# Performance work log

Measured on AMD Instinct MI355X. Metric: run time of the kernel, lower is better.

The kernel has to match this reference:

```python
import jax, jax.numpy as jnp
import numpy as np

B, T, D, U = 32, 1024, 512, 512

def hard_sigmoid(x):
    # Keras hard_sigmoid: clip(0.2*x + 0.5, 0, 1)
    return jnp.clip(x * 0.2 + 0.5, 0.0, 1.0)

def setup_inputs() -> dict:
    key = jax.random.key(0)
    k1, k2, k3 = jax.random.split(key, 3)
    x = jax.random.normal(k1, (B, T, D), dtype=jnp.float32)
    kernel = jax.random.normal(k2, (D, 4 * U), dtype=jnp.float32) * 0.02
    recurrent_kernel = jax.random.normal(k3, (U, 4 * U), dtype=jnp.float32) * 0.02
    # unit_forget_bias: forget-gate slice initialized to 1
    bias = jnp.zeros((4 * U,), dtype=jnp.float32).at[U:2 * U].set(1.0)
    return {"x": x, "kernel": kernel, "recurrent_kernel": recurrent_kernel, "bias": bias}

def reference(x, kernel, recurrent_kernel, bias):
    units = recurrent_kernel.shape[0]
    batch = x.shape[0]
    # Precompute input projections for all timesteps in one big GEMM
    # (implementation=2 style): [B, T, 4U]
    xz = jnp.einsum('btd,dg->btg', x, kernel) + bias
    xz_t = jnp.transpose(xz, (1, 0, 2))  # [T, B, 4U]

    h0 = jnp.zeros((batch, units), dtype=x.dtype)
    c0 = jnp.zeros((batch, units), dtype=x.dtype)

    def step(carry, z_x):
        h, c = carry
        z = z_x + h @ recurrent_kernel  # [B, 4U]
        zi, zf, zc, zo = jnp.split(z, 4, axis=-1)
        i = hard_sigmoid(zi)
        f = hard_sigmoid(zf)
        c_new = f * c + i * jnp.tanh(zc)
        o = hard_sigmoid(zo)
        h_new = o * jnp.tanh(c_new)
        return (h_new, c_new), h_new

    (_, _), hs = jax.lax.scan(step, (h0, c0), xz_t)  # hs: [T, B, U]
    return jnp.transpose(hs, (1, 0, 2))  # [B, T, U] (return_sequences=True)
```

## Files before the change

### kernel.cpp

```cpp
#include <hip/hip_runtime.h>


#define TT 1024
#define DD 512
#define UU 512
#define NCOL 2048
#define SENT 0xFFFFFFFFu
#define RDEPTH 4

typedef float f32x2 __attribute__((ext_vector_type(2)));
typedef float f32x4 __attribute__((ext_vector_type(4)));
typedef unsigned int u32x4 __attribute__((ext_vector_type(4)));

__device__ __forceinline__ float hsig(float v) {
  return fminf(fmaxf(0.2f * v + 0.5f, 0.0f), 1.0f);
}
__device__ __forceinline__ float tanh_fast(float x) {
  float e = __expf(2.0f * x);
  return 1.0f - 2.0f / (e + 1.0f);
}

template <bool SLEEP>
__device__ __forceinline__ void wavebar(int* ctr, int& ep) {
  asm volatile("s_waitcnt lgkmcnt(0)" ::: "memory");
  if ((threadIdx.x & 63) == 0)
    __hip_atomic_fetch_add(ctr, 1, __ATOMIC_RELAXED, __HIP_MEMORY_SCOPE_WORKGROUP);
  ep += 4;
  while (__hip_atomic_load(ctr, __ATOMIC_RELAXED, __HIP_MEMORY_SCOPE_WORKGROUP) < ep) {
    if (SLEEP) __builtin_amdgcn_s_sleep(1);
  }
  asm volatile("" ::: "memory");
}

__global__ __launch_bounds__(512, 2) void lstm_persistent(
    const float* __restrict__ x,
    const float* __restrict__ Wk,
    const float* __restrict__ Wr,
    const float* __restrict__ bias,
    float* __restrict__ out) {
  const int tid = (int)threadIdx.x;
  const int g   = (int)blockIdx.x & 7;
  const int w   = (int)blockIdx.x >> 3;
  const bool crit = (tid < 256);
  const int l   = tid & 63;

  __shared__ float LX[8][4][65];
  __shared__ float LR[2][8][4][66];
  __shared__ float RING[RDEPTH][4][66];
  __shared__ float LH[4][8][68];
  __shared__ float LB[64];
  __shared__ int cXZdone, cCRITdone, cXZbar, cCRITbar;

  if (tid == 0) { cXZdone = 0; cCRITdone = 0; cXZbar = 0; cCRITbar = 0; }
  if (tid < 64) LB[tid] = bias[(tid >> 4) * UU + w * 16 + (tid & 15)];

  f32x2 W2[64];
  {
    const int wv  = tid >> 6;
    const int idx = tid & 255;
    const int cp  = crit ? (l & 31) : (idx & 31);
    const int ko  = crit ? (2 * (wv & 3) + (l >> 5)) : (idx >> 5);
    const int gcb = (cp >> 3) * UU + w * 16 + ((2 * cp) & 15);
    const float* M = crit ? Wr : Wk;
#pragma unroll
    for (int j = 0; j < 64; ++j)
      W2[j] = *(const f32x2*)(M + (size_t)(64 * ko + j) * NCOL + gcb);
  }
  __syncthreads();

  if (crit) {
    const int wv   = tid >> 6;
    const int kq0  = 2 * wv;
    const int kql  = kq0 + (l >> 5);
    const int cp   = l & 31;
    const int gsel = l >> 4;
    const int b_p  = l >> 4;
    const int m    = l & 15;
    const unsigned* hb = (const unsigned*)out +
        (size_t)(g * 4 + b_p) * TT * UU + 128 * wv + 8 * m;
    float* lhdst = &LH[b_p][kq0 + (m >> 3)][8 * (m & 7)];
    float c_state = 0.0f;
    int epC = 0;

    for (int t = 0; t < TT; ++t) {
      if (t > 0) {
        const unsigned* p = hb + (size_t)(t - 1) * UU;
        u32x4 A, B;
        for (;;) {
          asm volatile(
              "global_load_dwordx4 %0, %2, off sc0 sc1\n\t"
              "global_load_dwordx4 %1, %2, off offset:16 sc0 sc1\n\t"
              "s_waitcnt vmcnt(0)"
              : "=v"(A), "=v"(B) : "v"(p) : "memory");
          int ok = (A.x != SENT) & (A.y != SENT) & (A.z != SENT) & (A.w != SENT) &
                   (B.x != SENT) & (B.y != SENT) & (B.z != SENT) & (B.w != SENT);
          if (__all(ok)) break;
          __builtin_amdgcn_s_sleep(1);
        }
        *(u32x4*)lhdst       = A;
        *(u32x4*)(lhdst + 4) = B;
        asm volatile("s_waitcnt lgkmcnt(0)" ::: "memory");
        __builtin_amdgcn_sched_barrier(0);
        __builtin_amdgcn_s_setprio(1);
        f32x2 a0 = {0.f, 0.f}, a1 = {0.f, 0.f}, a2 = {0.f, 0.f}, a3 = {0.f, 0.f};
#pragma unroll
        for (int j4 = 0; j4 < 16; ++j4) {
          f32x4 h0 = *(const f32x4*)&LH[0][kql][4 * j4];
          f32x4 h1 = *(const f32x4*)&LH[1][kql][4 * j4];
          f32x4 h2 = *(const f32x4*)&LH[2][kql][4 * j4];
          f32x4 h3 = *(const f32x4*)&LH[3][kql][4 * j4];
#pragma unroll
          for (int jj = 0; jj < 4; ++jj) {
            f32x2 wj = W2[4 * j4 + jj];
            a0 += (f32x2){h0[jj], h0[jj]} * wj;
            a1 += (f32x2){h1[jj], h1[jj]} * wj;
            a2 += (f32x2){h2[jj], h2[jj]} * wj;
            a3 += (f32x2){h3[jj], h3[jj]} * wj;
          }
        }
        __builtin_amdgcn_s_setprio(0);
        const int p2 = t & 1;
        *(f32x2*)&LR[p2][kql][0][2 * cp] = a0;
        *(f32x2*)&LR[p2][kql][1][2 * cp] = a1;
        *(f32x2*)&LR[p2][kql][2][2 * cp] = a2;
        *(f32x2*)&LR[p2][kql][3][2 * cp] = a3;
      }
      while (__hip_atomic_load(&cXZdone, __ATOMIC_RELAXED,
                               __HIP_MEMORY_SCOPE_WORKGROUP) < t + 1) {
      }
      asm volatile("" ::: "memory");
      float s = RING[t & (RDEPTH - 1)][wv][l] + LB[l];
      if (l == 0)
        __hip_atomic_fetch_add(&cCRITdone, 1, __ATOMIC_RELAXED,
                               __HIP_MEMORY_SCOPE_WORKGROUP);
      wavebar<false>(&cCRITbar, epC);
      if (t > 0) {
        const int p2 = t & 1;
#pragma unroll
        for (int kq = 0; kq < 8; ++kq) s += LR[p2][kq][wv][l];
      }
      float za  = __shfl_xor(s, 16);
      float zb  = __shfl_xor(s, 32);
      float zc2 = __shfl_xor(za, 32);
      float zi  = gsel == 0 ? s   : gsel == 1 ? za  : gsel == 2 ? zb  : zc2;
      float zf  = gsel == 0 ? za  : gsel == 1 ? s   : gsel == 2 ? zc2 : zb;
      float zc_ = gsel == 0 ? zb  : gsel == 1 ? zc2 : gsel == 2 ? s   : za;
      float zo  = gsel == 0 ? zc2 : gsel == 1 ? zb  : gsel == 2 ? za  : s;
      float gi = hsig(zi);
      float gf = hsig(zf);
      float gc = tanh_fast(zc_);
      float go = hsig(zo);
      c_state = gf * c_state + gi * gc;
      float h = go * tanh_fast(c_state);
      if (gsel == 0) {
        __hip_atomic_store(
            out + ((size_t)(g * 4 + wv) * TT + t) * UU + w * 16 + l, h,
            __ATOMIC_RELAXED, __HIP_MEMORY_SCOPE_AGENT);
      }
    }
  } else {
    const int idx = tid & 255;
    const int o   = idx >> 5;
    const int cp  = idx & 31;
    const float* xb0 = x + (size_t)(g * 4 + 0) * TT * DD + o * 64;
    const float* xb1 = x + (size_t)(g * 4 + 1) * TT * DD + o * 64;
    const float* xb2 = x + (size_t)(g * 4 + 2) * TT * DD + o * 64;
    const float* xb3 = x + (size_t)(g * 4 + 3) * TT * DD + o * 64;
    int epX = 0;

    for (int t = 0; t < TT; ++t) {
      const size_t off = (size_t)t * DD;
      f32x2 a0 = {0.f, 0.f}, a1 = {0.f, 0.f}, a2 = {0.f, 0.f}, a3 = {0.f, 0.f};
#pragma unroll
      for (int j4 = 0; j4 < 16; ++j4) {
        f32x4 v0 = *(const f32x4*)(xb0 + off + 4 * j4);
        f32x4 v1 = *(const f32x4*)(xb1 + off + 4 * j4);
        f32x4 v2 = *(const f32x4*)(xb2 + off + 4 * j4);
        f32x4 v3 = *(const f32x4*)(xb3 + off + 4 * j4);
#pragma unroll
        for (int jj = 0; jj < 4; ++jj) {
          f32x2 wj = W2[4 * j4 + jj];
          a0 += (f32x2){v0[jj], v0[jj]} * wj;
          a1 += (f32x2){v1[jj], v1[jj]} * wj;
          a2 += (f32x2){v2[jj], v2[jj]} * wj;
          a3 += (f32x2){v3[jj], v3[jj]} * wj;
        }
      }
      *(f32x2*)&LX[o][0][2 * cp] = a0;
      *(f32x2*)&LX[o][1][2 * cp] = a1;
      *(f32x2*)&LX[o][2][2 * cp] = a2;
      *(f32x2*)&LX[o][3][2 * cp] = a3;
      wavebar<true>(&cXZbar, epX);
      if (t >= RDEPTH) {
        while (__hip_atomic_load(&cCRITdone, __ATOMIC_RELAXED,
                                 __HIP_MEMORY_SCOPE_WORKGROUP) <
               4 * (t - RDEPTH + 1)) {
          __builtin_amdgcn_s_sleep(1);
        }
        asm volatile("" ::: "memory");
      }
      {
        const int b2 = idx >> 6, c3 = idx & 63;
        float ssum = 0.f;
#pragma unroll
        for (int oo = 0; oo < 8; ++oo) ssum += LX[oo][b2][c3];
        RING[t & (RDEPTH - 1)][b2][c3] = ssum;
      }
      wavebar<true>(&cXZbar, epX);
      if (idx == 0) {
        asm volatile("s_waitcnt lgkmcnt(0)" ::: "memory");
        __hip_atomic_fetch_add(&cXZdone, 1, __ATOMIC_RELAXED,
                               __HIP_MEMORY_SCOPE_WORKGROUP);
      }
    }
  }
}

extern "C" void kernel_launch(void* const* d_in, const int* in_sizes, int n_in,
                              void* d_out, int out_size, void* d_ws, size_t ws_size,
                              hipStream_t stream) {
  const float* x    = (const float*)d_in[0];
  const float* Wk   = (const float*)d_in[1];
  const float* Wr   = (const float*)d_in[2];
  const float* bias = (const float*)d_in[3];
  float* out = (float*)d_out;

  hipMemsetAsync(out, 0xFF, (size_t)out_size * sizeof(float), stream);
  lstm_persistent<<<256, 512, 0, stream>>>(x, Wk, Wr, bias, out);
}
```

Before: 4.792 ms.

## Split batch into two ping-pong halves to overlap h polling with recurrent compute

The four batch rows per block are split into two pairs processed alternately within each timestep, so the global load of one pair's previous hidden state is issued early and overlaps with the other pair's matvec and gate math. Hidden-state polling changes from per-thread dwordx4 loads to scattered dword loads issued ahead and drained with partial vmcnt waits. Gate computation now uses 16 lanes reading four gates directly instead of cross-lane shuffles. The input-projection producer is split per pair with separate counters. The cost is twice as many wave barriers per step and lower lane utilisation in the gate phase.

```diff
diff --git a/kernel.cpp b/kernel.cpp
--- a/kernel.cpp
+++ b/kernel.cpp
@@ -10,7 +10,6 @@
 
 typedef float f32x2 __attribute__((ext_vector_type(2)));
 typedef float f32x4 __attribute__((ext_vector_type(4)));
-typedef unsigned int u32x4 __attribute__((ext_vector_type(4)));
 
 __device__ __forceinline__ float hsig(float v) {
   return fminf(fmaxf(0.2f * v + 0.5f, 0.0f), 1.0f);
@@ -31,6 +30,38 @@
   }
   asm volatile("" ::: "memory");
 }
+
+#define ISSUE4(v0, v1, v2, v3, p0, p1)                                   \
+  asm volatile(                                                          \
+      "global_load_dword %0, %4, off sc0 sc1\n\t"                        \
+      "global_load_dword %1, %4, off offset:256 sc0 sc1\n\t"             \
+      "global_load_dword %2, %5, off sc0 sc1\n\t"                        \
+      "global_load_dword %3, %5, off offset:256 sc0 sc1"                 \
+      : "=v"(v0), "=v"(v1), "=v"(v2), "=v"(v3)                           \
+      : "v"(p0), "v"(p1)                                                 \
+      : "memory")
+
+#define DRAIN4(v0, v1, v2, v3)                                           \
+  asm volatile("s_waitcnt vmcnt(4)"                                      \
+               : "+v"(v0), "+v"(v1), "+v"(v2), "+v"(v3)::"memory")
+
+#define OK4(v0, v1, v2, v3)                                              \
+  ((v0 != SENT) & (v1 != SENT) & (v2 != SENT) & (v3 != SENT))
+
+#define REPOLL4(v0, v1, v2, v3, p0, p1)                                  \
+  for (;;) {                                                             \
+    asm volatile(                                                        \
+        "global_load_dword %0, %4, off sc0 sc1\n\t"                      \
+        "global_load_dword %1, %4, off offset:256 sc0 sc1\n\t"           \
+        "global_load_dword %2, %5, off sc0 sc1\n\t"                      \
+        "global_load_dword %3, %5, off offset:256 sc0 sc1\n\t"           \
+        "s_waitcnt vmcnt(0)"                                             \
+        : "=v"(v0), "=v"(v1), "=v"(v2), "=v"(v3)                         \
+        : "v"(p0), "v"(p1)                                               \
+        : "memory");                                                     \
+    if (__all(OK4(v0, v1, v2, v3))) break;                               \
+    __builtin_amdgcn_s_sleep(1);                                         \
+  }
 
 __global__ __launch_bounds__(512, 2) void lstm_persistent(
     const float* __restrict__ x,
@@ -44,14 +75,15 @@
   const bool crit = (tid < 256);
   const int l   = tid & 63;
 
-  __shared__ float LX[8][4][65];
-  __shared__ float LR[2][8][4][66];
-  __shared__ float RING[RDEPTH][4][66];
-  __shared__ float LH[4][8][68];
+  __shared__ float LX[8][2][66];
+  __shared__ float LR[2][2][8][2][66];
+  __shared__ float RING[2][RDEPTH][2][66];
+  __shared__ float LH[2][2][8][68];
   __shared__ float LB[64];
-  __shared__ int cXZdone, cCRITdone, cXZbar, cCRITbar;
-
-  if (tid == 0) { cXZdone = 0; cCRITdone = 0; cXZbar = 0; cCRITbar = 0; }
+  __shared__ int cXZdone[2], cCRITdone[2], cXZbar, cCRITbar;
+
+  if (tid < 2) { cXZdone[tid] = 0; cCRITdone[tid] = 0; }
+  if (tid == 0) { cXZbar = 0; cCRITbar = 0; }
   if (tid < 64) LB[tid] = bias[(tid >> 4) * UU + w * 16 + (tid & 15)];
 
   f32x2 W2[64];
@@ -73,144 +105,214 @@
     const int kq0  = 2 * wv;
     const int kql  = kq0 + (l >> 5);
     const int cp   = l & 31;
-    const int gsel = l >> 4;
-    const int b_p  = l >> 4;
-    const int m    = l & 15;
-    const unsigned* hb = (const unsigned*)out +
-        (size_t)(g * 4 + b_p) * TT * UU + 128 * wv + 8 * m;
-    float* lhdst = &LH[b_p][kq0 + (m >> 3)][8 * (m & 7)];
+    const int myp  = wv >> 1;
+    const int mybi = wv & 1;
+    const unsigned* oub[2][2];
+#pragma unroll
+    for (int p = 0; p < 2; ++p)
+#pragma unroll
+      for (int bi = 0; bi < 2; ++bi)
+        oub[p][bi] = (const unsigned*)out + (size_t)(g * 4 + 2 * p + bi) * TT * UU;
+    const size_t sl = 128 * wv + l;
     float c_state = 0.0f;
     int epC = 0;
+    unsigned sa0, sa1, sa2, sa3, sb0, sb1, sb2, sb3;
 
     for (int t = 0; t < TT; ++t) {
       if (t > 0) {
-        const unsigned* p = hb + (size_t)(t - 1) * UU;
-        u32x4 A, B;
-        for (;;) {
-          asm volatile(
-              "global_load_dwordx4 %0, %2, off sc0 sc1\n\t"
-              "global_load_dwordx4 %1, %2, off offset:16 sc0 sc1\n\t"
-              "s_waitcnt vmcnt(0)"
-              : "=v"(A), "=v"(B) : "v"(p) : "memory");
-          int ok = (A.x != SENT) & (A.y != SENT) & (A.z != SENT) & (A.w != SENT) &
-                   (B.x != SENT) & (B.y != SENT) & (B.z != SENT) & (B.w != SENT);
-          if (__all(ok)) break;
-          __builtin_amdgcn_s_sleep(1);
-        }
-        *(u32x4*)lhdst       = A;
-        *(u32x4*)(lhdst + 4) = B;
+        const size_t ro = (size_t)(t - 1) * UU + sl;
+        ISSUE4(sb0, sb1, sb2, sb3, oub[1][0] + ro, oub[1][1] + ro);
+      }
+      if (t > 0) {
+        const size_t ro = (size_t)(t - 1) * UU + sl;
+        DRAIN4(sa0, sa1, sa2, sa3);
+        if (!__all(OK4(sa0, sa1, sa2, sa3))) {
+          REPOLL4(sa0, sa1, sa2, sa3, oub[0][0] + ro, oub[0][1] + ro);
+        }
+        LH[0][0][kq0    ][l] = __uint_as_float(sa0);
+        LH[0][0][kq0 + 1][l] = __uint_as_float(sa1);
+        LH[0][1][kq0    ][l] = __uint_as_float(sa2);
+        LH[0][1][kq0 + 1][l] = __uint_as_float(sa3);
         asm volatile("s_waitcnt lgkmcnt(0)" ::: "memory");
         __builtin_amdgcn_sched_barrier(0);
         __builtin_amdgcn_s_setprio(1);
-        f32x2 a0 = {0.f, 0.f}, a1 = {0.f, 0.f}, a2 = {0.f, 0.f}, a3 = {0.f, 0.f};
+        f32x2 a0 = {0.f, 0.f}, a1 = {0.f, 0.f};
 #pragma unroll
         for (int j4 = 0; j4 < 16; ++j4) {
-          f32x4 h0 = *(const f32x4*)&LH[0][kql][4 * j4];
-          f32x4 h1 = *(const f32x4*)&LH[1][kql][4 * j4];
-          f32x4 h2 = *(const f32x4*)&LH[2][kql][4 * j4];
-          f32x4 h3 = *(const f32x4*)&LH[3][kql][4 * j4];
+          f32x4 h0 = *(const f32x4*)&LH[0][0][kql][4 * j4];
+          f32x4 h1 = *(const f32x4*)&LH[0][1][kql][4 * j4];
 #pragma unroll
           for (int jj = 0; jj < 4; ++jj) {
             f32x2 wj = W2[4 * j4 + jj];
             a0 += (f32x2){h0[jj], h0[jj]} * wj;
             a1 += (f32x2){h1[jj], h1[jj]} * wj;
-            a2 += (f32x2){h2[jj], h2[jj]} * wj;
-            a3 += (f32x2){h3[jj], h3[jj]} * wj;
           }
         }
         __builtin_amdgcn_s_setprio(0);
-        const int p2 = t & 1;
-        *(f32x2*)&LR[p2][kql][0][2 * cp] = a0;
-        *(f32x2*)&LR[p2][kql][1][2 * cp] = a1;
-        *(f32x2*)&LR[p2][kql][2][2 * cp] = a2;
-        *(f32x2*)&LR[p2][kql][3][2 * cp] = a3;
-      }
-      while (__hip_atomic_load(&cXZdone, __ATOMIC_RELAXED,
-                               __HIP_MEMORY_SCOPE_WORKGROUP) < t + 1) {
-      }
-      asm volatile("" ::: "memory");
-      float s = RING[t & (RDEPTH - 1)][wv][l] + LB[l];
-      if (l == 0)
-        __hip_atomic_fetch_add(&cCRITdone, 1, __ATOMIC_RELAXED,
-                               __HIP_MEMORY_SCOPE_WORKGROUP);
+        *(f32x2*)&LR[0][t & 1][kql][0][2 * cp] = a0;
+        *(f32x2*)&LR[0][t & 1][kql][1][2 * cp] = a1;
+      }
+      float s0 = 0.f, s1 = 0.f, s2 = 0.f, s3 = 0.f;
+      if (myp == 0 && l < 16) {
+        while (__hip_atomic_load(&cXZdone[0], __ATOMIC_RELAXED,
+                                 __HIP_MEMORY_SCOPE_WORKGROUP) < t + 1) {
+        }
+        asm volatile("" ::: "memory");
+        const int ss = t & (RDEPTH - 1);
+        s0 = RING[0][ss][mybi][l +  0] + LB[l +  0];
+        s1 = RING[0][ss][mybi][l + 16] + LB[l + 16];
+        s2 = RING[0][ss][mybi][l + 32] + LB[l + 32];
+        s3 = RING[0][ss][mybi][l + 48] + LB[l + 48];
+        if (wv == 0 && l == 0) {
+          asm volatile("s_waitcnt lgkmcnt(0)" ::: "memory");
+          __hip_atomic_fetch_add(&cCRITdone[0], 1, __ATOMIC_RELAXED,
+                                 __HIP_MEMORY_SCOPE_WORKGROUP);
+        }
+      }
       wavebar<false>(&cCRITbar, epC);
+      if (myp == 0 && l < 16) {
+        if (t > 0) {
+          const int par = t & 1;
+#pragma unroll
+          for (int kq = 0; kq < 8; ++kq) {
+            s0 += LR[0][par][kq][mybi][l +  0];
+            s1 += LR[0][par][kq][mybi][l + 16];
+            s2 += LR[0][par][kq][mybi][l + 32];
+            s3 += LR[0][par][kq][mybi][l + 48];
+          }
+        }
+        float gi = hsig(s0), gf = hsig(s1);
+        float gc = tanh_fast(s2), go = hsig(s3);
+        c_state = gf * c_state + gi * gc;
+        float h = go * tanh_fast(c_state);
+        __hip_atomic_store(
+            out + ((size_t)(g * 4 + mybi) * TT + t) * UU + w * 16 + l, h,
+            __ATOMIC_RELAXED, __HIP_MEMORY_SCOPE_AGENT);
+      }
+      {
+        const size_t ro = (size_t)t * UU + sl;
+        ISSUE4(sa0, sa1, sa2, sa3, oub[0][0] + ro, oub[0][1] + ro);
+      }
       if (t > 0) {
-        const int p2 = t & 1;
-#pragma unroll
-        for (int kq = 0; kq < 8; ++kq) s += LR[p2][kq][wv][l];
-      }
-      float za  = __shfl_xor(s, 16);
-      float zb  = __shfl_xor(s, 32);
-      float zc2 = __shfl_xor(za, 32);
-      float zi  = gsel == 0 ? s   : gsel == 1 ? za  : gsel == 2 ? zb  : zc2;
-      float zf  = gsel == 0 ? za  : gsel == 1 ? s   : gsel == 2 ? zc2 : zb;
-      float zc_ = gsel == 0 ? zb  : gsel == 1 ? zc2 : gsel == 2 ? s   : za;
-      float zo  = gsel == 0 ? zc2 : gsel == 1 ? zb  : gsel == 2 ? za  : s;
-      float gi = hsig(zi);
-      float gf = hsig(zf);
-      float gc = tanh_fast(zc_);
-      float go = hsig(zo);
-      c_state = gf * c_state + gi * gc;
-      float h = go * tanh_fast(c_state);
-      if (gsel == 0) {
+        const size_t ro = (size_t)(t - 1) * UU + sl;
+        DRAIN4(sb0, sb1, sb2, sb3);
+        if (!__all(OK4(sb0, sb1, sb2, sb3))) {
+          REPOLL4(sb0, sb1, sb2, sb3, oub[1][0] + ro, oub[1][1] + ro);
+        }
+        LH[1][0][kq0    ][l] = __uint_as_float(sb0);
+        LH[1][0][kq0 + 1][l] = __uint_as_float(sb1);
+        LH[1][1][kq0    ][l] = __uint_as_float(sb2);
+        LH[1][1][kq0 + 1][l] = __uint_as_float(sb3);
+        asm volatile("s_waitcnt lgkmcnt(0)" ::: "memory");
+        __builtin_amdgcn_sched_barrier(0);
+        __builtin_amdgcn_s_setprio(1);
+        f32x2 b0 = {0.f, 0.f}, b1 = {0.f, 0.f};
+#pragma unroll
+        for (int j4 = 0; j4 < 16; ++j4) {
+          f32x4 h0 = *(const f32x4*)&LH[1][0][kql][4 * j4];
+          f32x4 h1 = *(const f32x4*)&LH[1][1][kql][4 * j4];
+#pragma unroll
+          for (int jj = 0; jj < 4; ++jj) {
+            f32x2 wj = W2[4 * j4 + jj];
+            b0 += (f32x2){h0[jj], h0[jj]} * wj;
+            b1 += (f32x2){h1[jj], h1[jj]} * wj;
+          }
+        }
+        __builtin_amdgcn_s_setprio(0);
+        *(f32x2*)&LR[1][t & 1][kql][0][2 * cp] = b0;
+        *(f32x2*)&LR[1][t & 1][kql][1][2 * cp] = b1;
+      }
+      s0 = 0.f; s1 = 0.f; s2 = 0.f; s3 = 0.f;
+      if (myp == 1 && l < 16) {
+        while (__hip_atomic_load(&cXZdone[1], __ATOMIC_RELAXED,
+                                 __HIP_MEMORY_SCOPE_WORKGROUP) < t + 1) {
+        }
+        asm volatile("" ::: "memory");
+        const int ss = t & (RDEPTH - 1);
+        s0 = RING[1][ss][mybi][l +  0] + LB[l +  0];
+        s1 = RING[1][ss][mybi][l + 16] + LB[l + 16];
+        s2 = RING[1][ss][mybi][l + 32] + LB[l + 32];
+        s3 = RING[1][ss][mybi][l + 48] + LB[l + 48];
+        if (wv == 2 && l == 0) {
+          asm volatile("s_waitcnt lgkmcnt(0)" ::: "memory");
+          __hip_atomic_fetch_add(&cCRITdone[1], 1, __ATOMIC_RELAXED,
+                                 __HIP_MEMORY_SCOPE_WORKGROUP);
+        }
+      }
+      wavebar<false>(&cCRITbar, epC);
+      if (myp == 1 && l < 16) {
+        if (t > 0) {
+          const int par = t & 1;
+#pragma unroll
+          for (int kq = 0; kq < 8; ++kq) {
+            s0 += LR[1][par][kq][mybi][l +  0];
+            s1 += LR[1][par][kq][mybi][l + 16];
+            s2 += LR[1][par][kq][mybi][l + 32];
+            s3 += LR[1][par][kq][mybi][l + 48];
+          }
+        }
+        float gi = hsig(s0), gf = hsig(s1);
+        float gc = tanh_fast(s2), go = hsig(s3);
+        c_state = gf * c_state + gi * gc;
+        float h = go * tanh_fast(c_state);
         __hip_atomic_store(
-            out + ((size_t)(g * 4 + wv) * TT + t) * UU + w * 16 + l, h,
+            out + ((size_t)(g * 4 + 2 + mybi) * TT + t) * UU + w * 16 + l, h,
             __ATOMIC_RELAXED, __HIP_MEMORY_SCOPE_AGENT);
       }
     }
+    asm volatile("s_waitcnt vmcnt(0) lgkmcnt(0)" ::: "memory");
   } else {
     const int idx = tid & 255;
     const int o   = idx >> 5;
     const int cp  = idx & 31;
-    const float* xb0 = x + (size_t)(g * 4 + 0) * TT * DD + o * 64;
-    const float* xb1 = x + (size_t)(g * 4 + 1) * TT * DD + o * 64;
-    const float* xb2 = x + (size_t)(g * 4 + 2) * TT * DD + o * 64;
-    const float* xb3 = x + (size_t)(g * 4 + 3) * TT * DD + o * 64;
+    const float* xb[2][2];
+#pragma unroll
+    for (int p = 0; p < 2; ++p)
+#pragma unroll
+      for (int bi = 0; bi < 2; ++bi)
+        xb[p][bi] = x + (size_t)(g * 4 + 2 * p + bi) * TT * DD + o * 64;
     int epX = 0;
 
     for (int t = 0; t < TT; ++t) {
-      const size_t off = (size_t)t * DD;
-      f32x2 a0 = {0.f, 0.f}, a1 = {0.f, 0.f}, a2 = {0.f, 0.f}, a3 = {0.f, 0.f};
-#pragma unroll
-      for (int j4 = 0; j4 < 16; ++j4) {
-        f32x4 v0 = *(const f32x4*)(xb0 + off + 4 * j4);
-        f32x4 v1 = *(const f32x4*)(xb1 + off + 4 * j4);
-        f32x4 v2 = *(const f32x4*)(xb2 + off + 4 * j4);
-        f32x4 v3 = *(const f32x4*)(xb3 + off + 4 * j4);
-#pragma unroll
-        for (int jj = 0; jj < 4; ++jj) {
-          f32x2 wj = W2[4 * j4 + jj];
-          a0 += (f32x2){v0[jj], v0[jj]} * wj;
-          a1 += (f32x2){v1[jj], v1[jj]} * wj;
-          a2 += (f32x2){v2[jj], v2[jj]} * wj;
-          a3 += (f32x2){v3[jj], v3[jj]} * wj;
-        }
-      }
-      *(f32x2*)&LX[o][0][2 * cp] = a0;
-      *(f32x2*)&LX[o][1][2 * cp] = a1;
-      *(f32x2*)&LX[o][2][2 * cp] = a2;
-      *(f32x2*)&LX[o][3][2 * cp] = a3;
-      wavebar<true>(&cXZbar, epX);
-      if (t >= RDEPTH) {
-        while (__hip_atomic_load(&cCRITdone, __ATOMIC_RELAXED,
-                                 __HIP_MEMORY_SCOPE_WORKGROUP) <
-               4 * (t - RDEPTH + 1)) {
-          __builtin_amdgcn_s_sleep(1);
-        }
-        asm volatile("" ::: "memory");
-      }
-      {
-        const int b2 = idx >> 6, c3 = idx & 63;
-        float ssum = 0.f;
-#pragma unroll
-        for (int oo = 0; oo < 8; ++oo) ssum += LX[oo][b2][c3];
-        RING[t & (RDEPTH - 1)][b2][c3] = ssum;
-      }
-      wavebar<true>(&cXZbar, epX);
-      if (idx == 0) {
-        asm volatile("s_waitcnt lgkmcnt(0)" ::: "memory");
-        __hip_atomic_fetch_add(&cXZdone, 1, __ATOMIC_RELAXED,
-                               __HIP_MEMORY_SCOPE_WORKGROUP);
+#pragma unroll
+      for (int p = 0; p < 2; ++p) {
+        const size_t off = (size_t)t * DD;
+        f32x2 a0 = {0.f, 0.f}, a1 = {0.f, 0.f};
+#pragma unroll
+        for (int j4 = 0; j4 < 16; ++j4) {
+          f32x4 v0 = *(const f32x4*)(xb[p][0] + off + 4 * j4);
+          f32x4 v1 = *(const f32x4*)(xb[p][1] + off + 4 * j4);
+#pragma unroll
+          for (int jj = 0; jj < 4; ++jj) {
+            f32x2 wj = W2[4 * j4 + jj];
+            a0 += (f32x2){v0[jj], v0[jj]} * wj;
+            a1 += (f32x2){v1[jj], v1[jj]} * wj;
+          }
+        }
+        *(f32x2*)&LX[o][0][2 * cp] = a0;
+        *(f32x2*)&LX[o][1][2 * cp] = a1;
+        wavebar<true>(&cXZbar, epX);
+        if (t >= RDEPTH) {
+          while (__hip_atomic_load(&cCRITdone[p], __ATOMIC_RELAXED,
+                                   __HIP_MEMORY_SCOPE_WORKGROUP) <
+                 t - RDEPTH + 1) {
+            __builtin_amdgcn_s_sleep(1);
+          }
+          asm volatile("" ::: "memory");
+        }
+        if (idx < 128) {
+          const int bi = idx >> 6, c3 = idx & 63;
+          float ssum = 0.f;
+#pragma unroll
+          for (int oo = 0; oo < 8; ++oo) ssum += LX[oo][bi][c3];
+          RING[p][t & (RDEPTH - 1)][bi][c3] = ssum;
+        }
+        wavebar<true>(&cXZbar, epX);
+        if (idx == 0) {
+          asm volatile("s_waitcnt lgkmcnt(0)" ::: "memory");
+          __hip_atomic_fetch_add(&cXZdone[p], 1, __ATOMIC_RELAXED,
+                                 __HIP_MEMORY_SCOPE_WORKGROUP);
+        }
       }
     }
   }
```

Result: faster. 4.607 ms (-3.9%).
